# Kernel optimization log

Hardware: AMD Instinct MI355X
Metric: run time of the kernel (lower is better)

The kernel has to match this reference:

```python
import jax, jax.numpy as jnp
import numpy as np

RCR, RCA = 5.2, 3.5
ETA_R, ZETA, ETA_A = 16.0, 32.0, 8.0
SHF_R = 0.9 + 0.26875 * np.arange(16)            # 16 radial shifts
SHF_Z = (2.0 * np.arange(8) + 1.0) * np.pi / 16.0  # 8 angular shifts
SHF_A = 0.9 + 0.65 * np.arange(4)                # 4 angular-radial shifts
NUM_SPECIES = 4
_pm = np.zeros((NUM_SPECIES, NUM_SPECIES), np.int32)
_c = 0
for _s1 in range(NUM_SPECIES):
    for _s2 in range(_s1, NUM_SPECIES):
        _pm[_s1, _s2] = _pm[_s2, _s1] = _c
        _c += 1
PAIR_IDX = _pm  # unordered species pair -> 0..9 (torchani triu order)


def setup_inputs():
    key = jax.random.key(0)
    k1, k2 = jax.random.split(key)
    B, N = 512, 16
    species = jax.random.randint(k1, (B, N), 0, NUM_SPECIES)
    coordinates = jax.random.normal(k2, (B, N, 3), dtype=jnp.float32) * 2.0
    return {"species": species, "coordinates": coordinates}


def _aev(species, coordinates):
    B, N, _ = coordinates.shape
    dt = coordinates.dtype
    shfr = jnp.asarray(SHF_R, dt)
    shfz = jnp.asarray(SHF_Z, dt)
    shfa = jnp.asarray(SHF_A, dt)
    valid = species >= 0                                   # padding atoms have species = -1
    eye = jnp.eye(N, dtype=bool)
    pair_valid = valid[:, :, None] & valid[:, None, :] & ~eye          # [B,N,N]
    diff = coordinates[:, :, None, :] - coordinates[:, None, :, :]     # [B,N,N,3]
    d2 = jnp.sum(diff * diff, axis=-1)
    d = jnp.sqrt(jnp.where(pair_valid, d2, 1.0))                       # safe distances
    sp1h = jax.nn.one_hot(species, NUM_SPECIES, dtype=dt)              # [B,N,4]; zeros for padding

    # ---- radial AEV (cutoff Rcr) ----
    fcr = jnp.where(pair_valid & (d <= RCR), 0.5 * jnp.cos(jnp.pi * d / RCR) + 0.5, 0.0)
    rad = 0.25 * jnp.exp(-ETA_R * (d[..., None] - shfr) ** 2) * fcr[..., None]   # [B,N,N,16]
    radial_aev = jnp.einsum('bijr,bjs->bisr', rad, sp1h).reshape(B, N, NUM_SPECIES * 16)

    # ---- angular AEV (cutoff Rca) ----
    fca = jnp.where(pair_valid & (d <= RCA), 0.5 * jnp.cos(jnp.pi * d / RCA) + 0.5, 0.0)
    dot = jnp.einsum('bijx,bikx->bijk', diff, diff)                    # [B,N,N,N]
    cosang = jnp.clip(0.95 * dot / (d[:, :, :, None] * d[:, :, None, :]), -0.95, 0.95)
    ang = jnp.arccos(cosang)                                           # [B,N,N,N]
    f1 = ((1.0 + jnp.cos(ang[..., None] - shfz)) * 0.5) ** ZETA        # [B,N,N,N,8]
    davg = 0.5 * (d[:, :, :, None] + d[:, :, None, :])
    f2 = jnp.exp(-ETA_A * (davg[..., None] - shfa) ** 2)               # [B,N,N,N,4]
    tri = (fca[:, :, :, None] * fca[:, :, None, :]) * (~eye).astype(dt)[None, None]  # j != k
    # torchani subaev layout flattens (ShfA, ShfZ) -> 4*8 = 32
    ret = (tri[..., None, None] * f2[..., :, None] * f1[..., None, :]).reshape(B, N, N, N, 32)
    pair_oh = jax.nn.one_hot(jnp.asarray(PAIR_IDX), 10, dtype=dt)      # [4,4,10]
    w = jnp.einsum('bjs,bkt,stp->bjkp', sp1h, sp1h, pair_oh)           # [B,N,N,10]
    # torchani: 2*f1*f2*fc per UNORDERED pair; here ordered (j,k) double-counts -> net factor 1
    angular_aev = jnp.einsum('bijkf,bjkp->bipf', ret, w).reshape(B, N, 10 * 32)
    return jnp.concatenate([radial_aev, angular_aev], axis=-1)         # [B,N,384]


def reference(species, coordinates):
    return species, _aev(species, coordinates)
```

## Files before the change

### kernel.cpp

```cpp
#include <hip/hip_runtime.h>

#define NATOMS 16

__global__ __launch_bounds__(64, 8) void aev_kernel(const int* __restrict__ species,
                                                    const float* __restrict__ coords,
                                                    float* __restrict__ out,
                                                    int nmol) {
    const int l = threadIdx.x;
    const int bid = blockIdx.x;
    const int b = bid >> 4;
    const int i = bid & 15;

    __shared__ float scm[48];
    __shared__ int   ssp[16];
    __shared__ float dX[16], dY[16], dZ[16], sD[16], sRinv[16], sFca[16], sFcr4[16];
    __shared__ float rad[16][17];
    __shared__ int   hist[10], sBase[10], sCur[10];
    __shared__ float4 ebuf[105];

    if (l < 48) scm[l] = coords[b * 48 + l];
    if (l < 16) {
        int sp = species[b * 16 + l];
        ssp[l] = sp;
        if (i == 0) out[b * 16 + l] = (float)sp;
    }
    if (l < 10) hist[l] = 0;

    const int f = l & 31;
    const int z = f & 7, a = f >> 3;
    const float ang = (2.0f * (float)z + 1.0f) * 0.19634954084936207f;
    const float czh = 0.5f * __cosf(ang);
    const float szh = 0.5f * __sinf(ang);
    const float ga  = __expf(-3.38f * (float)(a * a - a));
    __syncthreads();

    const int spi = ssp[i];
    const float xi = scm[3 * i], yi = scm[3 * i + 1], zi = scm[3 * i + 2];

    if (l < 16) {
        const int jj = l;
        float dx = xi - scm[3 * jj], dy = yi - scm[3 * jj + 1], dz = zi - scm[3 * jj + 2];
        bool pv = (jj != i) && (spi >= 0) && (ssp[jj] >= 0);
        float d2 = dx * dx + dy * dy + dz * dz;
        float d = sqrtf(pv ? d2 : 1.0f);
        float rinv = 1.0f / d;
        float fca = (pv && d <= 3.5f) ? (0.5f * __cosf(d * 0.8975979010256552f) + 0.5f) : 0.0f;
        float fcr = (pv && d <= 5.2f) ? (0.5f * __cosf(d * 0.6041515809446141f) + 0.5f) : 0.0f;
        dX[jj] = dx; dY[jj] = dy; dZ[jj] = dz;
        sD[jj] = d; sRinv[jj] = rinv; sFca[jj] = fca; sFcr4[jj] = 0.25f * fcr;
    }
    __syncthreads();

    {
        const int jj = l & 15, rg = l >> 4;
        float d = sD[jj], f4 = sFcr4[jj];
        #pragma unroll
        for (int rr = 0; rr < 4; ++rr) {
            int r = rg * 4 + rr;
            float e = d - (0.9f + 0.26875f * (float)r);
            rad[jj][r] = f4 * __expf(-16.0f * e * e);
        }
    }

    int j1 = -1, k1 = -1, p1 = -1, j2 = -1, k2 = -1, p2 = -1;
    {
        int s = l;
        float sq = sqrtf((float)(961 - 8 * s));
        int j = (int)floorf((31.0f - sq) * 0.5f);
        j = j < 0 ? 0 : (j > 14 ? 14 : j);
        int off = (j * (31 - j)) >> 1;
        if (s < off) { --j; off = (j * (31 - j)) >> 1; }
        else { int off2 = ((j + 1) * (30 - j)) >> 1; if (s >= off2) { ++j; off = off2; } }
        int k = j + 1 + (s - off);
        if (sFca[j] > 0.f && sFca[k] > 0.f) {
            int s1 = ssp[j], s2 = ssp[k];
            int lo = s1 < s2 ? s1 : s2, hi = s1 < s2 ? s2 : s1;
            p1 = lo * 4 + hi - ((lo * (lo + 1)) >> 1);
            j1 = j; k1 = k;
            atomicAdd(&hist[p1], 1);
        }
    }
    if (l < 56) {
        int s = l + 64;
        float sq = sqrtf((float)(961 - 8 * s));
        int j = (int)floorf((31.0f - sq) * 0.5f);
        j = j < 0 ? 0 : (j > 14 ? 14 : j);
        int off = (j * (31 - j)) >> 1;
        if (s < off) { --j; off = (j * (31 - j)) >> 1; }
        else { int off2 = ((j + 1) * (30 - j)) >> 1; if (s >= off2) { ++j; off = off2; } }
        int k = j + 1 + (s - off);
        if (sFca[j] > 0.f && sFca[k] > 0.f) {
            int s1 = ssp[j], s2 = ssp[k];
            int lo = s1 < s2 ? s1 : s2, hi = s1 < s2 ? s2 : s1;
            p2 = lo * 4 + hi - ((lo * (lo + 1)) >> 1);
            j2 = j; k2 = k;
            atomicAdd(&hist[p2], 1);
        }
    }
    __syncthreads();

    if (l < 10) {
        int sum = 0;
        for (int qq = 0; qq < l; ++qq) sum += hist[qq];
        sBase[l] = sum;
        sCur[l] = sum;
    }
    __syncthreads();

    #pragma unroll
    for (int slot = 0; slot < 2; ++slot) {
        int jj = slot == 0 ? j1 : j2;
        int kk = slot == 0 ? k1 : k2;
        int pp = slot == 0 ? p1 : p2;
        if (jj >= 0) {
            float fj = sFca[jj], fk = sFca[kk];
            float dot = dX[jj] * dX[kk] + dY[jj] * dY[kk] + dZ[jj] * dZ[kk];
            float ca = 0.95f * dot * sRinv[jj] * sRinv[kk];
            ca = fminf(0.95f, fmaxf(-0.95f, ca));
            float sa = sqrtf(1.0f - ca * ca);
            float davg = 0.5f * (sD[jj] + sD[kk]);
            float e0 = davg - 0.9f;
            float t0 = 2.0f * fj * fk * __expf(-8.0f * e0 * e0);
            float r1 = __expf(10.4f * davg - 12.74f);
            int idx = atomicAdd(&sCur[pp], 1);
            ebuf[idx] = make_float4(ca, sa, t0, r1);
        }
    }
    __syncthreads();

    float* base_o = out + (size_t)nmol * 16 + (size_t)(b * 16 + i) * 384;
    {
        const int half = l >> 5;
        const bool a1 = (a & 1), a2 = (a & 2) != 0;
        #pragma unroll
        for (int pp = 0; pp < 5; ++pp) {
            int p = pp * 2 + half;
            int st = sBase[p];
            int n = hist[p];
            float acc = 0.0f;
            for (int e = 0; e < n; ++e) {
                float4 v = ebuf[st + e];
                float c1 = fmaf(czh, v.x, fmaf(szh, v.y, 0.5f));
                float c2 = c1 * c1;
                float c4 = c2 * c2;
                float c8 = c4 * c4;
                float c16 = c8 * c8;
                float c32 = c16 * c16;
                float tt = v.z;
                float rsq = v.w * v.w;
                tt = a1 ? tt * v.w : tt;
                tt = a2 ? tt * rsq : tt;
                acc = fmaf(tt, c32, acc);
            }
            base_o[64 + p * 32 + f] = acc * ga;
        }
    }

    {
        const int s_ = l >> 4, r_ = l & 15;
        float rv = 0.0f;
        #pragma unroll
        for (int jj = 0; jj < 16; ++jj)
            rv += (ssp[jj] == s_) ? rad[jj][r_] : 0.0f;
        base_o[l] = rv;
    }
}

extern "C" void kernel_launch(void* const* d_in, const int* in_sizes, int n_in,
                              void* d_out, int out_size, void* d_ws, size_t ws_size,
                              hipStream_t stream) {
    const int*   species = (const int*)d_in[0];
    const float* coords  = (const float*)d_in[1];
    float*       out     = (float*)d_out;
    int nmol = in_sizes[0] / NATOMS;
    aev_kernel<<<nmol * 16, 64, 0, stream>>>(species, coords, out, nmol);
}
```

Baseline: 70.86 us.

## Compact valid angular neighbors, batch four atoms per block, sparse radial sum

Each block now handles four center atoms, one per wavefront, so molecule data is loaded once per four atoms and the block count drops by four. A ballot builds a list of neighbours inside the angular cutoff, and triples are enumerated only over valid pairs. Geometry for each pair is computed once, before the histogram pass instead of after it. The radial species sum walks per-species ballot masks instead of testing all 16 neighbours, and sqrt/div are replaced by rsqrt. In exchange the kernel uses more shared memory per block and more per-wave bookkeeping.

```diff
diff --git a/kernel.cpp b/kernel.cpp
--- a/kernel.cpp
+++ b/kernel.cpp
@@ -1,33 +1,35 @@
 #include <hip/hip_runtime.h>
 
-#define NATOMS 16
+__global__ __launch_bounds__(256, 8) void aev_kernel(const int* __restrict__ species,
+                                                     const float* __restrict__ coords,
+                                                     float* __restrict__ out,
+                                                     int nmol) {
+    const int t = threadIdx.x;
+    const int w = t >> 6;
+    const int l = t & 63;
+    const int bid = blockIdx.x;
+    const int b = bid >> 2;
+    const int g = bid & 3;
+    const int i = g * 4 + w;
 
-__global__ __launch_bounds__(64, 8) void aev_kernel(const int* __restrict__ species,
-                                                    const float* __restrict__ coords,
-                                                    float* __restrict__ out,
-                                                    int nmol) {
-    const int l = threadIdx.x;
-    const int bid = blockIdx.x;
-    const int b = bid >> 4;
-    const int i = bid & 15;
+    __shared__ float  scm[48];
+    __shared__ int    ssp[16];
+    __shared__ float4 pd[4][16];
+    __shared__ float4 pf[4][16];
+    __shared__ float  rad[4][16][17];
+    __shared__ int    vlist[4][16];
+    __shared__ int    hist[4][10], sBase[4][10], sCur[4][10];
+    __shared__ float4 ebuf[4][105];
 
-    __shared__ float scm[48];
-    __shared__ int   ssp[16];
-    __shared__ float dX[16], dY[16], dZ[16], sD[16], sRinv[16], sFca[16], sFcr4[16];
-    __shared__ float rad[16][17];
-    __shared__ int   hist[10], sBase[10], sCur[10];
-    __shared__ float4 ebuf[105];
+    if (t < 48) scm[t] = coords[b * 48 + t];
+    if (t < 16) {
+        int sp = species[b * 16 + t];
+        ssp[t] = sp;
+        if (g == 0) out[b * 16 + t] = (float)sp;
+    }
+    if (l < 10) hist[w][l] = 0;
 
-    if (l < 48) scm[l] = coords[b * 48 + l];
-    if (l < 16) {
-        int sp = species[b * 16 + l];
-        ssp[l] = sp;
-        if (i == 0) out[b * 16 + l] = (float)sp;
-    }
-    if (l < 10) hist[l] = 0;
-
-    const int f = l & 31;
-    const int z = f & 7, a = f >> 3;
+    const int f = l & 31, z = f & 7, a = f >> 3;
     const float ang = (2.0f * (float)z + 1.0f) * 0.19634954084936207f;
     const float czh = 0.5f * __cosf(ang);
     const float szh = 0.5f * __sinf(ang);
@@ -37,95 +39,94 @@
     const int spi = ssp[i];
     const float xi = scm[3 * i], yi = scm[3 * i + 1], zi = scm[3 * i + 2];
 
+    int  spl = 0;
+    bool pvalid = false;
     if (l < 16) {
-        const int jj = l;
-        float dx = xi - scm[3 * jj], dy = yi - scm[3 * jj + 1], dz = zi - scm[3 * jj + 2];
-        bool pv = (jj != i) && (spi >= 0) && (ssp[jj] >= 0);
+        spl = ssp[l];
+        float dx = xi - scm[3 * l], dy = yi - scm[3 * l + 1], dz = zi - scm[3 * l + 2];
+        bool pv = (l != i) && (spi >= 0) && (spl >= 0);
         float d2 = dx * dx + dy * dy + dz * dz;
-        float d = sqrtf(pv ? d2 : 1.0f);
-        float rinv = 1.0f / d;
-        float fca = (pv && d <= 3.5f) ? (0.5f * __cosf(d * 0.8975979010256552f) + 0.5f) : 0.0f;
-        float fcr = (pv && d <= 5.2f) ? (0.5f * __cosf(d * 0.6041515809446141f) + 0.5f) : 0.0f;
-        dX[jj] = dx; dY[jj] = dy; dZ[jj] = dz;
-        sD[jj] = d; sRinv[jj] = rinv; sFca[jj] = fca; sFcr4[jj] = 0.25f * fcr;
+        float d2s = pv ? d2 : 1.0f;
+        float rinv = __frsqrt_rn(d2s);
+        float d = d2s * rinv;
+        float fca  = (pv && d <= 3.5f) ? fmaf(0.5f, __cosf(d * 0.8975979010256552f), 0.5f) : 0.0f;
+        float fcr4 = (pv && d <= 5.2f) ? 0.25f * fmaf(0.5f, __cosf(d * 0.6041515809446141f), 0.5f) : 0.0f;
+        pd[w][l] = make_float4(dx, dy, dz, d);
+        pf[w][l] = make_float4(rinv, fca, fcr4, 0.0f);
+        pvalid = fca > 0.0f;
     }
+    const unsigned long long vm = __ballot(pvalid);
+    const int V = __popcll(vm);
+    if (pvalid) {
+        int idx = __popcll(vm & ((1ull << l) - 1ull));
+        vlist[w][idx] = l | (spl << 4);
+    }
+    const unsigned m0 = (unsigned)__ballot(l < 16 && spl == 0);
+    const unsigned m1 = (unsigned)__ballot(l < 16 && spl == 1);
+    const unsigned m2 = (unsigned)__ballot(l < 16 && spl == 2);
+    const unsigned m3 = (unsigned)__ballot(l < 16 && spl == 3);
     __syncthreads();
 
     {
         const int jj = l & 15, rg = l >> 4;
-        float d = sD[jj], f4 = sFcr4[jj];
+        float d = pd[w][jj].w;
+        float fcr4 = pf[w][jj].z;
         #pragma unroll
         for (int rr = 0; rr < 4; ++rr) {
             int r = rg * 4 + rr;
             float e = d - (0.9f + 0.26875f * (float)r);
-            rad[jj][r] = f4 * __expf(-16.0f * e * e);
+            rad[w][jj][r] = fcr4 * __expf(-16.0f * e * e);
         }
     }
 
-    int j1 = -1, k1 = -1, p1 = -1, j2 = -1, k2 = -1, p2 = -1;
-    {
-        int s = l;
-        float sq = sqrtf((float)(961 - 8 * s));
-        int j = (int)floorf((31.0f - sq) * 0.5f);
-        j = j < 0 ? 0 : (j > 14 ? 14 : j);
-        int off = (j * (31 - j)) >> 1;
-        if (s < off) { --j; off = (j * (31 - j)) >> 1; }
-        else { int off2 = ((j + 1) * (30 - j)) >> 1; if (s >= off2) { ++j; off = off2; } }
-        int k = j + 1 + (s - off);
-        if (sFca[j] > 0.f && sFca[k] > 0.f) {
-            int s1 = ssp[j], s2 = ssp[k];
-            int lo = s1 < s2 ? s1 : s2, hi = s1 < s2 ? s2 : s1;
-            p1 = lo * 4 + hi - ((lo * (lo + 1)) >> 1);
-            j1 = j; k1 = k;
-            atomicAdd(&hist[p1], 1);
-        }
-    }
-    if (l < 56) {
-        int s = l + 64;
-        float sq = sqrtf((float)(961 - 8 * s));
-        int j = (int)floorf((31.0f - sq) * 0.5f);
-        j = j < 0 ? 0 : (j > 14 ? 14 : j);
-        int off = (j * (31 - j)) >> 1;
-        if (s < off) { --j; off = (j * (31 - j)) >> 1; }
-        else { int off2 = ((j + 1) * (30 - j)) >> 1; if (s >= off2) { ++j; off = off2; } }
-        int k = j + 1 + (s - off);
-        if (sFca[j] > 0.f && sFca[k] > 0.f) {
-            int s1 = ssp[j], s2 = ssp[k];
-            int lo = s1 < s2 ? s1 : s2, hi = s1 < s2 ? s2 : s1;
-            p2 = lo * 4 + hi - ((lo * (lo + 1)) >> 1);
-            j2 = j; k2 = k;
-            atomicAdd(&hist[p2], 1);
+    const int nt = (V * (V - 1)) >> 1;
+    const int tw = 2 * V - 1;
+    float ca0 = 0.f, sa0 = 0.f, t00 = 0.f, r10 = 0.f; int p0 = -1;
+    float ca1 = 0.f, sa1 = 0.f, t01 = 0.f, r11 = 0.f; int p1 = -1;
+    #pragma unroll
+    for (int slot = 0; slot < 2; ++slot) {
+        const int s = slot == 0 ? l : (64 + l);
+        if (s < nt) {
+            float disc = (float)(tw * tw - 8 * s);
+            int aa = (int)floorf(0.5f * ((float)tw - sqrtf(disc)));
+            aa = aa < 0 ? 0 : (aa > V - 2 ? V - 2 : aa);
+            int offa = (aa * (2 * V - 1 - aa)) >> 1;
+            if (s < offa) { --aa; offa = (aa * (2 * V - 1 - aa)) >> 1; }
+            else { int offn = ((aa + 1) * (2 * V - 2 - aa)) >> 1; if (s >= offn) { ++aa; offa = offn; } }
+            const int bb = aa + 1 + (s - offa);
+            const int va = vlist[w][aa], vb = vlist[w][bb];
+            const int j = va & 15, spj = va >> 4;
+            const int k = vb & 15, spk = vb >> 4;
+            float4 Pj = pd[w][j], Pk = pd[w][k];
+            float4 Fj = pf[w][j], Fk = pf[w][k];
+            float dot = Pj.x * Pk.x + Pj.y * Pk.y + Pj.z * Pk.z;
+            float ca = 0.95f * dot * Fj.x * Fk.x;
+            ca = fminf(0.95f, fmaxf(-0.95f, ca));
+            float s2 = 1.0f - ca * ca;
+            float sa = s2 * __frsqrt_rn(s2);
+            float davg = 0.5f * (Pj.w + Pk.w);
+            float e0 = davg - 0.9f;
+            float t0 = 2.0f * Fj.y * Fk.y * __expf(-8.0f * e0 * e0);
+            float r1 = __expf(10.4f * davg - 12.74f);
+            int lo = spj < spk ? spj : spk, hi = spj < spk ? spk : spj;
+            int p = lo * 4 + hi - ((lo * (lo + 1)) >> 1);
+            atomicAdd(&hist[w][p], 1);
+            if (slot == 0) { ca0 = ca; sa0 = sa; t00 = t0; r10 = r1; p0 = p; }
+            else           { ca1 = ca; sa1 = sa; t01 = t0; r11 = r1; p1 = p; }
         }
     }
     __syncthreads();
 
     if (l < 10) {
         int sum = 0;
-        for (int qq = 0; qq < l; ++qq) sum += hist[qq];
-        sBase[l] = sum;
-        sCur[l] = sum;
+        for (int qq = 0; qq < l; ++qq) sum += hist[w][qq];
+        sBase[w][l] = sum;
+        sCur[w][l] = sum;
     }
     __syncthreads();
 
-    #pragma unroll
-    for (int slot = 0; slot < 2; ++slot) {
-        int jj = slot == 0 ? j1 : j2;
-        int kk = slot == 0 ? k1 : k2;
-        int pp = slot == 0 ? p1 : p2;
-        if (jj >= 0) {
-            float fj = sFca[jj], fk = sFca[kk];
-            float dot = dX[jj] * dX[kk] + dY[jj] * dY[kk] + dZ[jj] * dZ[kk];
-            float ca = 0.95f * dot * sRinv[jj] * sRinv[kk];
-            ca = fminf(0.95f, fmaxf(-0.95f, ca));
-            float sa = sqrtf(1.0f - ca * ca);
-            float davg = 0.5f * (sD[jj] + sD[kk]);
-            float e0 = davg - 0.9f;
-            float t0 = 2.0f * fj * fk * __expf(-8.0f * e0 * e0);
-            float r1 = __expf(10.4f * davg - 12.74f);
-            int idx = atomicAdd(&sCur[pp], 1);
-            ebuf[idx] = make_float4(ca, sa, t0, r1);
-        }
-    }
+    if (p0 >= 0) { int idx = atomicAdd(&sCur[w][p0], 1); ebuf[w][idx] = make_float4(ca0, sa0, t00, r10); }
+    if (p1 >= 0) { int idx = atomicAdd(&sCur[w][p1], 1); ebuf[w][idx] = make_float4(ca1, sa1, t01, r11); }
     __syncthreads();
 
     float* base_o = out + (size_t)nmol * 16 + (size_t)(b * 16 + i) * 384;
@@ -135,11 +136,11 @@
         #pragma unroll
         for (int pp = 0; pp < 5; ++pp) {
             int p = pp * 2 + half;
-            int st = sBase[p];
-            int n = hist[p];
+            int st = sBase[w][p];
+            int n = hist[w][p];
             float acc = 0.0f;
             for (int e = 0; e < n; ++e) {
-                float4 v = ebuf[st + e];
+                float4 v = ebuf[w][st + e];
                 float c1 = fmaf(czh, v.x, fmaf(szh, v.y, 0.5f));
                 float c2 = c1 * c1;
                 float c4 = c2 * c2;
@@ -158,10 +159,13 @@
 
     {
         const int s_ = l >> 4, r_ = l & 15;
+        unsigned m = s_ < 2 ? (s_ == 0 ? m0 : m1) : (s_ == 2 ? m2 : m3);
         float rv = 0.0f;
-        #pragma unroll
-        for (int jj = 0; jj < 16; ++jj)
-            rv += (ssp[jj] == s_) ? rad[jj][r_] : 0.0f;
+        while (m) {
+            int jj = __ffs(m) - 1;
+            m &= m - 1;
+            rv += rad[w][jj][r_];
+        }
         base_o[l] = rv;
     }
 }
@@ -172,6 +176,6 @@
     const int*   species = (const int*)d_in[0];
     const float* coords  = (const float*)d_in[1];
     float*       out     = (float*)d_out;
-    int nmol = in_sizes[0] / NATOMS;
-    aev_kernel<<<nmol * 16, 64, 0, stream>>>(species, coords, out, nmol);
+    int nmol = in_sizes[0] / 16;
+    aev_kernel<<<nmol * 4, 256, 0, stream>>>(species, coords, out, nmol);
 }
```

Result: faster. 68.09 us (-3.9%).
